# Kernel tuning notes

Measured on AMD Instinct MI355X. Metric: run time of the kernel, lower is better.

Reference implementation:

```python
import jax, jax.numpy as jnp
import numpy as np
from itertools import permutations

N = 4            # n_streams
C = 2048         # hidden_size
NC = N * C
NFACT = 24       # 4!
DFF = 4 * C
B, S = 2, 4096
EPS = 1.1920929e-07  # torch F.rms_norm default eps = finfo(fp32).eps


def _perm_mat():
    perms = list(permutations(range(N)))
    P = np.zeros((len(perms), N * N), np.float32)
    for i, p in enumerate(perms):
        for r, c in enumerate(p):
            P[i, r * N + c] = 1.0
    return jnp.asarray(P)


def setup_inputs() -> dict:
    key = jax.random.key(0)
    ks = jax.random.split(key, 8)
    total_out = 2 * N + NFACT
    return {
        "x_streams": jax.random.normal(ks[0], (B, S, N, C), jnp.float32),
        "W_all": jax.random.normal(ks[1], (total_out, NC), jnp.float32) * (1.0 / np.sqrt(NC)),
        "b_all": jax.random.normal(ks[2], (total_out,), jnp.float32) * 0.02,
        "alpha_pre": jnp.array([0.01], jnp.float32),
        "alpha_post": jnp.array([0.01], jnp.float32),
        "alpha_res": jnp.array([0.01], jnp.float32),
        "W1": jax.random.normal(ks[3], (DFF, C), jnp.float32) * (1.0 / np.sqrt(C)),
        "b1": jnp.zeros((DFF,), jnp.float32),
        "W2": jax.random.normal(ks[4], (C, DFF), jnp.float32) * (1.0 / np.sqrt(DFF)),
        "b2": jnp.zeros((C,), jnp.float32),
        "perm_mat": _perm_mat(),
    }


def reference(x_streams, W_all, b_all, alpha_pre, alpha_post, alpha_res, W1, b1, W2, b2, perm_mat):
    # --- coefficients: fused RMSNorm + projection + gating ---
    x_flat = x_streams.reshape(*x_streams.shape[:-2], NC)            # (B,S,nC)
    x_norm = x_flat * jax.lax.rsqrt(jnp.mean(x_flat * x_flat, axis=-1, keepdims=True) + EPS)
    all_proj = x_norm @ W_all.T                                       # (B,S,2n+n!)
    pre_proj = all_proj[..., :N]
    post_proj = all_proj[..., N:2 * N]
    res_proj = all_proj[..., 2 * N:]
    h_pre = jax.nn.sigmoid(alpha_pre * pre_proj + b_all[:N])          # (B,S,n)
    h_post = 2.0 * jax.nn.sigmoid(alpha_post * post_proj + b_all[N:2 * N])
    a_res = jax.nn.softmax(alpha_res * res_proj + b_all[2 * N:], axis=-1)  # (B,S,n!)
    H_res = (a_res @ perm_mat).reshape(*a_res.shape[:-1], N, N)       # (B,S,n,n)
    H_merged = H_res - h_post[..., :, None] * h_pre[..., None, :]
    # --- pre-map: weighted sum over streams ---
    layer_input = jnp.einsum('bsn,bsnc->bsc', h_pre, x_streams)       # (B,S,C)
    # --- wrapped layer: GELU MLP (no residual) ---
    h = jax.nn.gelu(layer_input @ W1.T + b1, approximate=False)
    layer_output = h @ W2.T + b2                                      # (B,S,C)
    # --- post-res mixing ---
    out = jnp.einsum('bsij,bsjc->bsic', H_merged, x_streams) \
        + h_post[..., None] * layer_output[..., None, :]
    return out
```

## Files before the change

kernel.cpp:

```cpp
#include <hip/hip_runtime.h>
#include <hip/hip_bf16.h>
#include <math.h>

#define NC_DIM 8192
#define C_DIM 2048
#define NTOK 8192
#define EPS_RMS 1.1920929e-07f

typedef __bf16 bf16_t;
typedef __attribute__((ext_vector_type(8))) __bf16 bf16x8;
typedef __attribute__((ext_vector_type(4))) __bf16 bf16x4;
typedef __attribute__((ext_vector_type(4))) float f32x4;

__device__ __forceinline__ void gload_lds16(const void* g, void* l) {
    __builtin_amdgcn_global_load_lds(
        (const __attribute__((address_space(1))) void*)g,
        (__attribute__((address_space(3))) void*)l, 16, 0, 0);
}

__global__ __launch_bounds__(256) void cvt_f32_bf16(const float* __restrict__ in,
                                                    bf16_t* __restrict__ out,
                                                    const int n4) {
    int i = blockIdx.x * 256 + threadIdx.x;
    const int stride = gridDim.x * 256;
    for (; i < n4; i += stride) {
        f32x4 v = ((const f32x4*)in)[i];
        bf16x4 bv;
        bv.x = (__bf16)v.x; bv.y = (__bf16)v.y; bv.z = (__bf16)v.z; bv.w = (__bf16)v.w;
        ((bf16x4*)out)[i] = bv;
    }
}

__global__ __launch_bounds__(256) void k_proj(
    const float* __restrict__ x,
    const float* __restrict__ Wall,
    const float* __restrict__ ball,
    const float* __restrict__ apre,
    const float* __restrict__ apost,
    const float* __restrict__ ares,
    const float* __restrict__ perm,
    float* __restrict__ hpre_g,
    float* __restrict__ hpost_g,
    float* __restrict__ Hm_g)
{
    __shared__ __align__(16) bf16_t xs[32 * 264];
    __shared__ __align__(16) bf16_t wsl[32 * 264];
    __shared__ float dparts[4][32][32];
    __shared__ float ssq_s[32];
    __shared__ float Ps[384];

    const int t = threadIdx.x;
    const int lane = t & 63;
    const int w = t >> 6;
    const int tok0 = blockIdx.x * 32;

    for (int i = t; i < 384; i += 256) Ps[i] = perm[i];

    const int row = t >> 3;
    const int i8 = t & 7;

    const float* xrow = x + (size_t)(tok0 + row) * (size_t)NC_DIM;
    const float* wrow = Wall + (size_t)row * (size_t)NC_DIM;

    float ssq = 0.0f;
    f32x4 acc[2][2];
#pragma unroll
    for (int m = 0; m < 2; ++m)
#pragma unroll
        for (int n = 0; n < 2; ++n) acc[m][n] = (f32x4){0.f, 0.f, 0.f, 0.f};

    const int rsel = lane & 15;
    const int ko_base = (lane >> 4) * 8;

    for (int kt = 0; kt < NC_DIM; kt += 256) {
        __syncthreads();
#pragma unroll
        for (int q = 0; q < 8; ++q) {
            const int col = (i8 + q * 8) * 4;
            f32x4 v = *(const f32x4*)(xrow + kt + col);
            ssq += v.x * v.x + v.y * v.y + v.z * v.z + v.w * v.w;
            bf16x4 bv;
            bv.x = (__bf16)v.x; bv.y = (__bf16)v.y; bv.z = (__bf16)v.z; bv.w = (__bf16)v.w;
            *(bf16x4*)(xs + row * 264 + col) = bv;
            f32x4 u = *(const f32x4*)(wrow + kt + col);
            bf16x4 bu;
            bu.x = (__bf16)u.x; bu.y = (__bf16)u.y; bu.z = (__bf16)u.z; bu.w = (__bf16)u.w;
            *(bf16x4*)(wsl + row * 264 + col) = bu;
        }
        __syncthreads();
#pragma unroll
        for (int ks = 0; ks < 2; ++ks) {
            const int ko = w * 64 + ks * 32 + ko_base;
            bf16x8 a0 = *(const bf16x8*)(xs + rsel * 264 + ko);
            bf16x8 a1 = *(const bf16x8*)(xs + (16 + rsel) * 264 + ko);
            bf16x8 b0 = *(const bf16x8*)(wsl + rsel * 264 + ko);
            bf16x8 b1 = *(const bf16x8*)(wsl + (16 + rsel) * 264 + ko);
            acc[0][0] = __builtin_amdgcn_mfma_f32_16x16x32_bf16(a0, b0, acc[0][0], 0, 0, 0);
            acc[0][1] = __builtin_amdgcn_mfma_f32_16x16x32_bf16(a0, b1, acc[0][1], 0, 0, 0);
            acc[1][0] = __builtin_amdgcn_mfma_f32_16x16x32_bf16(a1, b0, acc[1][0], 0, 0, 0);
            acc[1][1] = __builtin_amdgcn_mfma_f32_16x16x32_bf16(a1, b1, acc[1][1], 0, 0, 0);
        }
    }

    ssq += __shfl_xor(ssq, 1);
    ssq += __shfl_xor(ssq, 2);
    ssq += __shfl_xor(ssq, 4);
    if (i8 == 0) ssq_s[row] = ssq;

    const int cr = (lane >> 4) * 4;
#pragma unroll
    for (int m = 0; m < 2; ++m)
#pragma unroll
        for (int n = 0; n < 2; ++n)
#pragma unroll
            for (int j = 0; j < 4; ++j)
                dparts[w][m * 16 + cr + j][n * 16 + rsel] = acc[m][n][j];
    __syncthreads();

    if (t < 32) {
        const int g = tok0 + t;
        const float rinv = rsqrtf(ssq_s[t] * (1.0f / (float)NC_DIM) + EPS_RMS);
        float proj[32];
#pragma unroll
        for (int r = 0; r < 32; ++r)
            proj[r] = (dparts[0][t][r] + dparts[1][t][r] + dparts[2][t][r] + dparts[3][t][r]) * rinv;
        const float aP = apre[0], aQ = apost[0], aR = ares[0];
        float hp[4], hq[4];
#pragma unroll
        for (int i = 0; i < 4; ++i) {
            hp[i] = 1.0f / (1.0f + expf(-(aP * proj[i] + __ldg(&ball[i]))));
            hq[i] = 2.0f / (1.0f + expf(-(aQ * proj[4 + i] + __ldg(&ball[4 + i]))));
        }
        float zb[24];
        float mx = -1e30f;
#pragma unroll
        for (int p = 0; p < 24; ++p) {
            zb[p] = aR * proj[8 + p] + __ldg(&ball[8 + p]);
            mx = fmaxf(mx, zb[p]);
        }
        float s = 0.f;
#pragma unroll
        for (int p = 0; p < 24; ++p) { zb[p] = expf(zb[p] - mx); s += zb[p]; }
        const float is = 1.0f / s;
        float Hr[16];
#pragma unroll
        for (int idx = 0; idx < 16; ++idx) Hr[idx] = 0.f;
#pragma unroll
        for (int p = 0; p < 24; ++p) {
            const float a = zb[p] * is;
#pragma unroll
            for (int idx = 0; idx < 16; ++idx) Hr[idx] += a * Ps[p * 16 + idx];
        }
#pragma unroll
        for (int i = 0; i < 4; ++i) {
            hpre_g[(size_t)g * 4 + i] = hp[i];
            hpost_g[(size_t)g * 4 + i] = hq[i];
#pragma unroll
            for (int j = 0; j < 4; ++j)
                Hm_g[(size_t)g * 16 + i * 4 + j] = Hr[i * 4 + j] - hq[i] * hp[j];
        }
    }
}

__global__ __launch_bounds__(256) void k_mix(
    const float* __restrict__ x,
    const float* __restrict__ hpre_g,
    bf16_t* __restrict__ li)
{
    __shared__ float hp[8][4];
    const int t = threadIdx.x;
    const size_t tok0 = (size_t)blockIdx.x * 8;
    if (t < 32) hp[t >> 2][t & 3] = hpre_g[tok0 * 4 + t];
    __syncthreads();
    const int tl = t >> 5;
    const int ci = (t & 31) * 4;
    const size_t g = tok0 + tl;
    const float* xb = x + g * (size_t)NC_DIM;
    bf16_t* lo = li + g * (size_t)C_DIM;
    const float h0 = hp[tl][0], h1 = hp[tl][1], h2 = hp[tl][2], h3 = hp[tl][3];
#pragma unroll
    for (int q = 0; q < 16; ++q) {
        const int c = ci + q * 128;
        f32x4 v0 = *(const f32x4*)(xb + c);
        f32x4 v1 = *(const f32x4*)(xb + 2048 + c);
        f32x4 v2 = *(const f32x4*)(xb + 4096 + c);
        f32x4 v3 = *(const f32x4*)(xb + 6144 + c);
        f32x4 r = h0 * v0 + h1 * v1 + h2 * v2 + h3 * v3;
        bf16x4 bv;
        bv.x = (__bf16)r.x; bv.y = (__bf16)r.y; bv.z = (__bf16)r.z; bv.w = (__bf16)r.w;
        *(bf16x4*)(lo + c) = bv;
    }
}

template <int MODE>
__global__ __launch_bounds__(512, 2) void gemm8(
    const bf16_t* __restrict__ A,
    const bf16_t* __restrict__ Bm,
    const float* __restrict__ bias,
    void* __restrict__ Cout,
    const int M, const int N, const int K)
{
    __shared__ __align__(16) char lds[131072];
    const int tid = threadIdx.x;
    const int lane = tid & 63;
    const int w = tid >> 6;
    const int wr = w >> 2;
    const int wc = w & 3;

    const int nbn = N >> 8;
    const int cpx = gridDim.x >> 3;
    const int bid = blockIdx.x;
    const int swz = (bid & 7) * cpx + (bid >> 3);
    const long tm = (long)(swz / nbn) * 256;
    const long tn = (long)(swz % nbn) * 256;

    const int NT = K >> 6;

    const int rsel = lane & 15;
    const int ko = (lane >> 4) * 8;
    const int lane_off = rsel * 64 + ((ko ^ (((rsel >> 1) & 3) << 3)) << 1);

    const char* Abytes = (const char*)A;
    const char* Bbytes = (const char*)Bm;
    size_t asrc[2][2], bsrc[2][2];
#pragma unroll
    for (int i = 0; i < 2; ++i) {
        const int d = i * 8192 + tid * 16;
        {
            const int awr = d >> 13, rem = d & 8191;
            const int sub = rem >> 10, rs = sub >> 1, ksub = sub & 1;
            const int rr = (rem >> 6) & 15;
            const int kk = ((rem & 63) >> 1) ^ (((rr >> 1) & 3) << 3);
            const int k = ksub * 32 + kk;
#pragma unroll
            for (int mq = 0; mq < 2; ++mq) {
                const long grow = tm + awr * 128 + mq * 64 + rs * 16 + rr;
                asrc[mq][i] = ((size_t)grow * K + k) * 2;
            }
        }
        {
            const int bwc = d >> 12, rem = d & 4095;
            const int sub = rem >> 10, rs = sub >> 1, ksub = sub & 1;
            const int rr = (rem >> 6) & 15;
            const int kk = ((rem & 63) >> 1) ^ (((rr >> 1) & 3) << 3);
            const int k = ksub * 32 + kk;
#pragma unroll
            for (int np = 0; np < 2; ++np) {
                const long grow = tn + bwc * 64 + np * 32 + rs * 16 + rr;
                bsrc[np][i] = ((size_t)grow * K + k) * 2;
            }
        }
    }

    auto stageA = [&](int mq, int tile, int slot) {
        const int tt = tile < NT ? tile : NT - 1;
        char* dst = lds + slot * 65536 + mq * 16384 + w * 1024;
        gload_lds16(Abytes + asrc[mq][0] + (size_t)tt * 128, dst);
        gload_lds16(Abytes + asrc[mq][1] + (size_t)tt * 128, dst + 8192);
    };
    auto stageB = [&](int np, int tile, int slot) {
        const int tt = tile < NT ? tile : NT - 1;
        char* dst = lds + slot * 65536 + 32768 + np * 16384 + w * 1024;
        gload_lds16(Bbytes + bsrc[np][0] + (size_t)tt * 128, dst);
        gload_lds16(Bbytes + bsrc[np][1] + (size_t)tt * 128, dst + 8192);
    };

    const char* aB = lds + wr * 8192;
    const char* bB = lds + 32768 + wc * 4096;

    f32x4 acc[8][4];
#pragma unroll
    for (int m = 0; m < 8; ++m)
#pragma unroll
        for (int n = 0; n < 4; ++n) acc[m][n] = (f32x4){0.f, 0.f, 0.f, 0.f};

    bf16x8 aR[4][2], b01[2][2], b23[2][2];

    stageA(0, 0, 0); stageB(0, 0, 0); stageB(1, 0, 0); stageA(1, 0, 0);
    stageA(0, 1, 1); stageB(0, 1, 1); stageB(1, 1, 1);
    asm volatile("s_waitcnt vmcnt(6)" ::: "memory");
    __builtin_amdgcn_s_barrier();

    for (int t = 0; t < NT; ++t) {
        const int s = t & 1;
        const char* aS = aB + s * 65536;
        const char* bS = bB + s * 65536;
#pragma unroll
        for (int mf = 0; mf < 4; ++mf)
#pragma unroll
            for (int ks = 0; ks < 2; ++ks)
                aR[mf][ks] = *(const bf16x8*)(aS + (mf * 2 + ks) * 1024 + lane_off);
#pragma unroll
        for (int nf = 0; nf < 2; ++nf)
#pragma unroll
            for (int ks = 0; ks < 2; ++ks) {
                b01[nf][ks] = *(const bf16x8*)(bS + (nf * 2 + ks) * 1024 + lane_off);
                b23[nf][ks] = *(const bf16x8*)(bS + 16384 + (nf * 2 + ks) * 1024 + lane_off);
            }
        stageA(1, t + 1, s ^ 1);
        __builtin_amdgcn_s_setprio(1);
#pragma unroll
        for (int ks = 0; ks < 2; ++ks)
#pragma unroll
            for (int mf = 0; mf < 4; ++mf)
#pragma unroll
                for (int nf = 0; nf < 2; ++nf) {
                    acc[mf][nf] = __builtin_amdgcn_mfma_f32_16x16x32_bf16(aR[mf][ks], b01[nf][ks], acc[mf][nf], 0, 0, 0);
                    acc[mf][2 + nf] = __builtin_amdgcn_mfma_f32_16x16x32_bf16(aR[mf][ks], b23[nf][ks], acc[mf][2 + nf], 0, 0, 0);
                }
        __builtin_amdgcn_s_setprio(0);
        __builtin_amdgcn_s_barrier();
#pragma unroll
        for (int mf = 0; mf < 4; ++mf)
#pragma unroll
            for (int ks = 0; ks < 2; ++ks)
                aR[mf][ks] = *(const bf16x8*)(aS + 16384 + (mf * 2 + ks) * 1024 + lane_off);
        stageA(0, t + 2, s);
        stageB(0, t + 2, s);
        stageB(1, t + 2, s);
        asm volatile("s_waitcnt vmcnt(6)" ::: "memory");
        __builtin_amdgcn_s_setprio(1);
#pragma unroll
        for (int ks = 0; ks < 2; ++ks)
#pragma unroll
            for (int mf = 0; mf < 4; ++mf)
#pragma unroll
                for (int nf = 0; nf < 2; ++nf) {
                    acc[4 + mf][2 + nf] = __builtin_amdgcn_mfma_f32_16x16x32_bf16(aR[mf][ks], b23[nf][ks], acc[4 + mf][2 + nf], 0, 0, 0);
                    acc[4 + mf][nf] = __builtin_amdgcn_mfma_f32_16x16x32_bf16(aR[mf][ks], b01[nf][ks], acc[4 + mf][nf], 0, 0, 0);
                }
        __builtin_amdgcn_s_setprio(0);
        __builtin_amdgcn_s_barrier();
    }

#pragma unroll
    for (int mq = 0; mq < 2; ++mq)
#pragma unroll
        for (int mf = 0; mf < 4; ++mf) {
            const long rbase = tm + wr * 128 + mq * 64 + mf * 16 + (lane >> 4) * 4;
#pragma unroll
            for (int np = 0; np < 2; ++np)
#pragma unroll
                for (int nf = 0; nf < 2; ++nf) {
                    const long cg = tn + wc * 64 + np * 32 + nf * 16 + rsel;
                    const float bv = __ldg(&bias[cg]);
                    const f32x4 v4 = acc[mq * 4 + mf][np * 2 + nf];
#pragma unroll
                    for (int j = 0; j < 4; ++j) {
                        const float v = v4[j] + bv;
                        if (MODE == 0) {
                            const float ge = 0.5f * v * (1.0f + erff(v * 0.70710678118654752f));
                            ((bf16_t*)Cout)[(size_t)(rbase + j) * N + cg] = (__bf16)ge;
                        } else {
                            ((float*)Cout)[(size_t)(rbase + j) * N + cg] = v;
                        }
                    }
                }
        }
}

__global__ __launch_bounds__(256) void k_final(
    const float* __restrict__ x,
    const float* __restrict__ LO,
    const float* __restrict__ hpost_g,
    const float* __restrict__ Hm_g,
    float* __restrict__ out)
{
    __shared__ float Hm[16];
    __shared__ float hp[4];
    const int t = threadIdx.x;
    const size_t g = blockIdx.x;
    if (t < 16) Hm[t] = Hm_g[g * 16 + t];
    if (t >= 16 && t < 20) hp[t - 16] = hpost_g[g * 4 + (t - 16)];
    __syncthreads();
    const float* xb = x + g * (size_t)NC_DIM;
    const float* lob = LO + g * (size_t)C_DIM;
    float* ob = out + g * (size_t)NC_DIM;
#pragma unroll
    for (int q = 0; q < 2; ++q) {
        const int c = t * 4 + q * 1024;
        f32x4 x0 = *(const f32x4*)(xb + c);
        f32x4 x1 = *(const f32x4*)(xb + 2048 + c);
        f32x4 x2 = *(const f32x4*)(xb + 4096 + c);
        f32x4 x3 = *(const f32x4*)(xb + 6144 + c);
        f32x4 l4 = *(const f32x4*)(lob + c);
#pragma unroll
        for (int i = 0; i < 4; ++i) {
            f32x4 r = Hm[i * 4 + 0] * x0 + Hm[i * 4 + 1] * x1 + Hm[i * 4 + 2] * x2 +
                      Hm[i * 4 + 3] * x3 + hp[i] * l4;
            *(f32x4*)(ob + i * 2048 + c) = r;
        }
    }
}

extern "C" void kernel_launch(void* const* d_in, const int* in_sizes, int n_in,
                              void* d_out, int out_size, void* d_ws, size_t ws_size,
                              hipStream_t stream) {
    const float* x     = (const float*)d_in[0];
    const float* Wall  = (const float*)d_in[1];
    const float* ball  = (const float*)d_in[2];
    const float* apre  = (const float*)d_in[3];
    const float* apost = (const float*)d_in[4];
    const float* ares  = (const float*)d_in[5];
    const float* W1    = (const float*)d_in[6];
    const float* b1    = (const float*)d_in[7];
    const float* W2    = (const float*)d_in[8];
    const float* b2    = (const float*)d_in[9];
    const float* perm  = (const float*)d_in[10];
    float* out = (float*)d_out;
    char* ws = (char*)d_ws;

    bf16_t* W1b  = (bf16_t*)(ws);
    bf16_t* W2b  = (bf16_t*)(ws + 33554432ull);
    bf16_t* li   = (bf16_t*)(ws + 67108864ull);
    bf16_t* h    = (bf16_t*)(ws + 100663296ull);
    float*  LO   = (float*)(ws + 234881024ull);
    float*  hpre = (float*)(ws + 301989888ull);
    float*  hpost= (float*)(ws + 302120960ull);
    float*  Hm   = (float*)(ws + 302252032ull);

    cvt_f32_bf16<<<2048, 256, 0, stream>>>(W1, W1b, 16777216 / 4);
    cvt_f32_bf16<<<2048, 256, 0, stream>>>(W2, W2b, 16777216 / 4);
    k_proj<<<256, 256, 0, stream>>>(x, Wall, ball, apre, apost, ares, perm, hpre, hpost, Hm);
    k_mix<<<1024, 256, 0, stream>>>(x, hpre, li);
    gemm8<0><<<1024, 512, 0, stream>>>(li, W1b, b1, (void*)h, 8192, 8192, 2048);
    gemm8<1><<<256, 512, 0, stream>>>(h, W2b, b2, (void*)LO, 8192, 2048, 8192);
    k_final<<<8192, 256, 0, stream>>>(x, LO, hpost, Hm, out);
}
```

Baseline: 841.6 us.

## Restructure GEMM main loop into finer-grained eight-phase ping-pong schedule

Rewrites the bf16 MFMA GEMM main loop as a two-tile unrolled iteration split into eight phases. Each phase interleaves LDS reads, a global-to-LDS stage and a quarter of the MFMAs, separated by barriers and explicit lgkmcnt/vmcnt waits. The aim is to overlap LDS and global traffic with matrix math more evenly across waves, in the style of HipKittens. In exchange it adds many more barriers, assumes NT is even, and the per-phase issue order of the stageA/stageB slots differs from before.

```diff
diff --git a/kernel.cpp b/kernel.cpp
--- a/kernel.cpp
+++ b/kernel.cpp
@@ -276,62 +276,103 @@
 
     bf16x8 aR[4][2], b01[2][2], b23[2][2];
 
+    auto readA = [&](const char* aS, int off) {
+#pragma unroll
+        for (int mf = 0; mf < 4; ++mf)
+#pragma unroll
+            for (int ks = 0; ks < 2; ++ks)
+                aR[mf][ks] = *(const bf16x8*)(aS + off + (mf * 2 + ks) * 1024 + lane_off);
+    };
+    auto readB = [&](bf16x8 (&bf)[2][2], const char* bS, int off) {
+#pragma unroll
+        for (int nf = 0; nf < 2; ++nf)
+#pragma unroll
+            for (int ks = 0; ks < 2; ++ks)
+                bf[nf][ks] = *(const bf16x8*)(bS + off + (nf * 2 + ks) * 1024 + lane_off);
+    };
+
+#define MFMA_Q(MBASE, NBASE, BF)                                                   \
+    __builtin_amdgcn_s_setprio(1);                                                 \
+    _Pragma("unroll")                                                              \
+    for (int ks = 0; ks < 2; ++ks)                                                 \
+        _Pragma("unroll")                                                          \
+        for (int mf = 0; mf < 4; ++mf)                                             \
+            _Pragma("unroll")                                                      \
+            for (int nf = 0; nf < 2; ++nf)                                         \
+                acc[(MBASE) + mf][(NBASE) + nf] =                                  \
+                    __builtin_amdgcn_mfma_f32_16x16x32_bf16(                       \
+                        aR[mf][ks], BF[nf][ks], acc[(MBASE) + mf][(NBASE) + nf],   \
+                        0, 0, 0);                                                  \
+    __builtin_amdgcn_s_setprio(0);
+
+#define BAR() __builtin_amdgcn_s_barrier()
+#define LGKM0() asm volatile("s_waitcnt lgkmcnt(0)" ::: "memory")
+#define LGKM8() asm volatile("s_waitcnt lgkmcnt(8)" ::: "memory")
+#define VM6() asm volatile("s_waitcnt vmcnt(6)" ::: "memory")
+
     stageA(0, 0, 0); stageB(0, 0, 0); stageB(1, 0, 0); stageA(1, 0, 0);
     stageA(0, 1, 1); stageB(0, 1, 1); stageB(1, 1, 1);
-    asm volatile("s_waitcnt vmcnt(6)" ::: "memory");
-    __builtin_amdgcn_s_barrier();
-
-    for (int t = 0; t < NT; ++t) {
-        const int s = t & 1;
-        const char* aS = aB + s * 65536;
-        const char* bS = bB + s * 65536;
-#pragma unroll
-        for (int mf = 0; mf < 4; ++mf)
-#pragma unroll
-            for (int ks = 0; ks < 2; ++ks)
-                aR[mf][ks] = *(const bf16x8*)(aS + (mf * 2 + ks) * 1024 + lane_off);
-#pragma unroll
-        for (int nf = 0; nf < 2; ++nf)
-#pragma unroll
-            for (int ks = 0; ks < 2; ++ks) {
-                b01[nf][ks] = *(const bf16x8*)(bS + (nf * 2 + ks) * 1024 + lane_off);
-                b23[nf][ks] = *(const bf16x8*)(bS + 16384 + (nf * 2 + ks) * 1024 + lane_off);
-            }
-        stageA(1, t + 1, s ^ 1);
-        __builtin_amdgcn_s_setprio(1);
-#pragma unroll
-        for (int ks = 0; ks < 2; ++ks)
-#pragma unroll
-            for (int mf = 0; mf < 4; ++mf)
-#pragma unroll
-                for (int nf = 0; nf < 2; ++nf) {
-                    acc[mf][nf] = __builtin_amdgcn_mfma_f32_16x16x32_bf16(aR[mf][ks], b01[nf][ks], acc[mf][nf], 0, 0, 0);
-                    acc[mf][2 + nf] = __builtin_amdgcn_mfma_f32_16x16x32_bf16(aR[mf][ks], b23[nf][ks], acc[mf][2 + nf], 0, 0, 0);
-                }
-        __builtin_amdgcn_s_setprio(0);
-        __builtin_amdgcn_s_barrier();
-#pragma unroll
-        for (int mf = 0; mf < 4; ++mf)
-#pragma unroll
-            for (int ks = 0; ks < 2; ++ks)
-                aR[mf][ks] = *(const bf16x8*)(aS + 16384 + (mf * 2 + ks) * 1024 + lane_off);
-        stageA(0, t + 2, s);
-        stageB(0, t + 2, s);
-        stageB(1, t + 2, s);
-        asm volatile("s_waitcnt vmcnt(6)" ::: "memory");
-        __builtin_amdgcn_s_setprio(1);
-#pragma unroll
-        for (int ks = 0; ks < 2; ++ks)
-#pragma unroll
-            for (int mf = 0; mf < 4; ++mf)
-#pragma unroll
-                for (int nf = 0; nf < 2; ++nf) {
-                    acc[4 + mf][2 + nf] = __builtin_amdgcn_mfma_f32_16x16x32_bf16(aR[mf][ks], b23[nf][ks], acc[4 + mf][2 + nf], 0, 0, 0);
-                    acc[4 + mf][nf] = __builtin_amdgcn_mfma_f32_16x16x32_bf16(aR[mf][ks], b01[nf][ks], acc[4 + mf][nf], 0, 0, 0);
-                }
-        __builtin_amdgcn_s_setprio(0);
-        __builtin_amdgcn_s_barrier();
-    }
+    VM6();
+    BAR();
+
+    const int NI = NT >> 1;
+    for (int it = 0; it < NI; ++it) {
+        const int T = it * 2;
+        const char* aS0 = aB;
+        const char* bS0 = bB;
+        const char* aS1 = aB + 65536;
+        const char* bS1 = bB + 65536;
+
+        readA(aS0, 0);
+        readB(b01, bS0, 0);
+        stageA(1, T + 1, 1);
+        LGKM8();
+        BAR(); LGKM0();
+        MFMA_Q(0, 0, b01)
+        BAR();
+        readB(b23, bS0, 16384);
+        stageA(0, T + 2, 0);
+        BAR(); LGKM0();
+        MFMA_Q(0, 2, b23)
+        BAR();
+        readA(aS0, 16384);
+        stageB(0, T + 2, 0);
+        BAR(); LGKM0();
+        MFMA_Q(4, 2, b23)
+        BAR();
+        stageB(1, T + 2, 0);
+        VM6();
+        BAR();
+        MFMA_Q(4, 0, b01)
+        BAR();
+        readA(aS1, 0);
+        readB(b01, bS1, 0);
+        stageA(1, T + 2, 0);
+        LGKM8();
+        BAR(); LGKM0();
+        MFMA_Q(0, 0, b01)
+        BAR();
+        readB(b23, bS1, 16384);
+        stageA(0, T + 3, 1);
+        BAR(); LGKM0();
+        MFMA_Q(0, 2, b23)
+        BAR();
+        readA(aS1, 16384);
+        stageB(0, T + 3, 1);
+        BAR(); LGKM0();
+        MFMA_Q(4, 2, b23)
+        BAR();
+        stageB(1, T + 3, 1);
+        VM6();
+        BAR();
+        MFMA_Q(4, 0, b01)
+        BAR();
+    }
+#undef MFMA_Q
+#undef BAR
+#undef LGKM0
+#undef LGKM8
+#undef VM6
 
 #pragma unroll
     for (int mq = 0; mq < 2; ++mq)
```

New measurement: 829.4 us. No clear change (-1.4%).
